# Kernel tuning notes

Measured on AMD Instinct MI355X. Metric: run time of the kernel, lower is better.

## Reference

```python
import jax, jax.numpy as jnp
import numpy as np

N_NODES = 100000
N_EDGES = 1000000
D_IN = 64
D_OUT = 64


def setup_inputs() -> dict:
    key = jax.random.key(0)
    k1, k2, k3, k4 = jax.random.split(key, 4)
    x = jax.random.normal(k1, (N_NODES, D_IN), dtype=jnp.float32)
    edge_index = jax.random.randint(k2, (2, N_EDGES), 0, N_NODES, dtype=jnp.int64)
    edge_weight = jax.random.uniform(k3, (N_EDGES,), dtype=jnp.float32)
    W = jax.random.normal(k4, (D_OUT, D_IN), dtype=jnp.float32) * (1.0 / np.sqrt(D_IN))
    bias = jnp.zeros((D_OUT,), dtype=jnp.float32)
    return {"x": x, "edge_index": edge_index, "edge_weight": edge_weight, "W": W, "bias": bias}


def reference(x, edge_index, edge_weight, W, bias):
    n = x.shape[0]
    self_loops = jnp.arange(n)
    row = jnp.concatenate([edge_index[0], self_loops])  # [E+N]
    col = jnp.concatenate([edge_index[1], self_loops])  # [E+N]
    ew = jnp.concatenate([edge_weight, jnp.ones((n,), x.dtype)])  # [E+N]
    # degree via scatter-add of edge weights into row nodes
    deg = jax.ops.segment_sum(ew, row, num_segments=n)  # [N]
    deg_safe = jnp.where(deg > 0, deg, 1.0)
    deg_inv_sqrt = jnp.where(deg > 0, jax.lax.rsqrt(deg_safe), 0.0)  # inf -> 0
    norm = deg_inv_sqrt[row] * ew * deg_inv_sqrt[col]  # [E+N]
    # gather-scale-scatter aggregation
    msg = x[col] * norm[:, None]  # [E+N, D_IN]
    out = jax.ops.segment_sum(msg, row, num_segments=n)  # [N, D_IN]
    return out @ W.T + bias
```

## Files before the change

kernel.cpp:

```cpp
#include <hip/hip_runtime.h>
#include <hip/hip_bf16.h>

#define D 64
#define K 24
#define M44 ((1ULL << 44) - 1)
#define SPILLCAP 65536

__global__ __launch_bounds__(256) void k_build(const int* __restrict__ rowi,
                                               const int* __restrict__ coli,
                                               const float* __restrict__ ew,
                                               unsigned long long* __restrict__ packed,
                                               unsigned int* __restrict__ slots,
                                               int4* __restrict__ spill,
                                               int* __restrict__ spillCnt, int nE) {
    int e = blockIdx.x * 256 + threadIdx.x;
    if (e >= nE) return;
    int r = rowi[e];
    int c = coli[e];
    float w = ew[e];
    unsigned long long fx = (unsigned long long)((double)w * 4294967296.0);
    unsigned long long old = atomicAdd(&packed[r], (1ULL << 44) | fx);
    int rank = (int)(old >> 44);
    if (rank < K) {
        int q = (int)(w * 32768.0f + 0.5f);
        if (q > 32767) q = 32767;
        slots[r * K + rank] = ((unsigned int)c << 15) | (unsigned int)q;
    } else {
        int p = atomicAdd(spillCnt, 1);
        if (p < SPILLCAP) spill[p] = make_int4(r, c, __float_as_int(w), 0);
    }
}

__global__ __launch_bounds__(256) void k_dis(const unsigned long long* __restrict__ packed,
                                             float* __restrict__ dis,
                                             int* __restrict__ cnt, int n) {
    int i = blockIdx.x * 256 + threadIdx.x;
    if (i >= n) return;
    unsigned long long p = packed[i];
    float dg = (float)(1.0 + (double)(p & M44) * (1.0 / 4294967296.0));
    dis[i] = rsqrtf(dg);
    cnt[i] = (int)(p >> 44);
}

__global__ __launch_bounds__(256) void k_gather_gemm(const float* __restrict__ x,
                                                     const float* __restrict__ dis,
                                                     const int* __restrict__ cnt,
                                                     const unsigned int* __restrict__ slots,
                                                     const int4* __restrict__ spill,
                                                     const int* __restrict__ spillCnt,
                                                     const float* __restrict__ W,
                                                     const float* __restrict__ bias,
                                                     float* __restrict__ out, int n) {
    __shared__ float Bs[D * D];
    __shared__ float Ast[16 * D];
    float4* Ast4 = (float4*)Ast;
    int tid = threadIdx.x;

    const float4* W4 = (const float4*)W;
#pragma unroll
    for (int v = 0; v < 4; ++v) {
        int idx = tid + v * 256;
        int o  = idx >> 4;
        int kc = idx & 15;
        float4 wv = W4[idx];
        int gq = o >> 2, oo = o & 3;
        { int k = 4 * kc + 0; Bs[k * 64 + 4 * ((gq + k) & 15) + oo] = wv.x; }
        { int k = 4 * kc + 1; Bs[k * 64 + 4 * ((gq + k) & 15) + oo] = wv.y; }
        { int k = 4 * kc + 2; Bs[k * 64 + 4 * ((gq + k) & 15) + oo] = wv.z; }
        { int k = 4 * kc + 3; Bs[k * 64 + 4 * ((gq + k) & 15) + oo] = wv.w; }
    }

    int j   = tid & 15;
    int grp = tid >> 4;
    int i0  = blockIdx.x * 16;
    int i   = i0 + grp;

    float4 acc = make_float4(0.f, 0.f, 0.f, 0.f);
    const float4* x4 = (const float4*)x;
    if (i < n) {
        int rawc = cnt[i];
        int c_n = rawc < K ? rawc : K;
        int s = i * K;
        for (int off = 0; off < c_n; off += 16) {
            int idx = off + j;
            unsigned int rec = 0u;
            float wj = 0.f;
            if (idx < c_n) {
                rec = slots[s + idx];
                wj = (float)(rec & 32767u) * (1.0f / 32768.0f) * dis[rec >> 15];
            }
            int mm = c_n - off; if (mm > 16) mm = 16;
#pragma unroll
            for (int t = 0; t < 16; ++t) {
                if (t < mm) {
                    int col = (int)((unsigned int)__shfl((int)rec, t, 16) >> 15);
                    float w = __shfl(wj, t, 16);
                    float4 xv = x4[col * 16 + j];
                    acc.x += w * xv.x; acc.y += w * xv.y;
                    acc.z += w * xv.z; acc.w += w * xv.w;
                }
            }
        }
        if (rawc > K) {
            int total = *spillCnt;
            if (total > SPILLCAP) total = SPILLCAP;
            for (int sp = 0; sp < total; ++sp) {
                int4 v = spill[sp];
                if (v.x == i) {
                    float w = __int_as_float(v.z) * dis[v.y];
                    float4 xv = x4[v.y * 16 + j];
                    acc.x += w * xv.x; acc.y += w * xv.y;
                    acc.z += w * xv.z; acc.w += w * xv.w;
                }
            }
        }
        float di = dis[i];
        float4 xi = x4[i * 16 + j];
        acc.x = di * (di * xi.x + acc.x);
        acc.y = di * (di * xi.y + acc.y);
        acc.z = di * (di * xi.z + acc.z);
        acc.w = di * (di * xi.w + acc.w);
    }
    Ast4[grp * 16 + ((j + (grp >> 2)) & 15)] = acc;
    __syncthreads();

    int row = tid >> 4;
    int cg  = tid & 15;
    float4 oacc = ((const float4*)bias)[cg];
#pragma unroll 4
    for (int kc = 0; kc < 16; ++kc) {
        float4 a4 = Ast4[row * 16 + ((kc + (row >> 2)) & 15)];
        float4 b0 = *(const float4*)&Bs[(4 * kc + 0) * 64 + 4 * ((cg + 4 * kc + 0) & 15)];
        float4 b1 = *(const float4*)&Bs[(4 * kc + 1) * 64 + 4 * ((cg + 4 * kc + 1) & 15)];
        float4 b2 = *(const float4*)&Bs[(4 * kc + 2) * 64 + 4 * ((cg + 4 * kc + 2) & 15)];
        float4 b3 = *(const float4*)&Bs[(4 * kc + 3) * 64 + 4 * ((cg + 4 * kc + 3) & 15)];
        oacc.x += a4.x * b0.x + a4.y * b1.x + a4.z * b2.x + a4.w * b3.x;
        oacc.y += a4.x * b0.y + a4.y * b1.y + a4.z * b2.y + a4.w * b3.y;
        oacc.z += a4.x * b0.z + a4.y * b1.z + a4.z * b2.z + a4.w * b3.z;
        oacc.w += a4.x * b0.w + a4.y * b1.w + a4.z * b2.w + a4.w * b3.w;
    }
    int r = i0 + row;
    if (r < n) ((float4*)out)[r * 16 + cg] = oacc;
}

extern "C" void kernel_launch(void* const* d_in, const int* in_sizes, int n_in,
                              void* d_out, int out_size, void* d_ws, size_t ws_size,
                              hipStream_t stream) {
    const float* x    = (const float*)d_in[0];
    const int*   ei   = (const int*)d_in[1];
    const float* ew   = (const float*)d_in[2];
    const float* W    = (const float*)d_in[3];
    const float* bias = (const float*)d_in[4];
    float* out = (float*)d_out;

    int n  = in_sizes[0] / D;
    int nE = in_sizes[2];
    const int* rowi = ei;
    const int* coli = ei + nE;

    char* w = (char*)d_ws;
    unsigned long long* packed = (unsigned long long*)w; w += (size_t)n * 8;
    int* spillCnt = (int*)w;                             w += 64;
    unsigned int* slots = (unsigned int*)w;              w += (size_t)n * K * 4;
    float* dis = (float*)w;                              w += (size_t)n * 4;
    int*   cnt = (int*)w;                                w += (size_t)n * 4;
    int4*  spill = (int4*)w;

    int gn = (n + 255) / 256;
    int gE = (nE + 255) / 256;
    int gT = (n + 15) / 16;

    hipMemsetAsync(packed, 0, (size_t)n * 8 + 64, stream);
    k_build<<<gE, 256, 0, stream>>>(rowi, coli, ew, packed, slots, spill, spillCnt, nE);
    k_dis  <<<gn, 256, 0, stream>>>(packed, dis, cnt, n);
    k_gather_gemm<<<gT, 256, 0, stream>>>(x, dis, cnt, slots, spill, spillCnt, W, bias, out, n);
}
```

Before: 213.3 us.

## Fuse build, degree and gather-GEMM stages into one cooperative persistent kernel

Replaces the memset plus three separate kernel launches with a single cooperative kernel. It clears the workspace, builds the slot table with atomics, computes degree normalization, and runs the gather plus 64x64 GEMM over persistent tiles, with grid-wide syncs between phases. The goal is to remove per-launch and inter-kernel gaps, and to load W into shared memory once per block instead of once per tile. In exchange it adds grid.sync overhead, caps the grid to occupancy-limited size, and changes how work is spread across blocks. A fallback to the old multi-kernel path remains if the cooperative launch fails.

```diff
diff --git a/kernel.cpp b/kernel.cpp
--- a/kernel.cpp
+++ b/kernel.cpp
@@ -1,10 +1,148 @@
 #include <hip/hip_runtime.h>
+#include <hip/hip_cooperative_groups.h>
 #include <hip/hip_bf16.h>
 
 #define D 64
 #define K 24
 #define M44 ((1ULL << 44) - 1)
 #define SPILLCAP 65536
+
+namespace cg = cooperative_groups;
+
+struct FParams {
+    const float* x; const int* rowi; const int* coli; const float* ew;
+    const float* W; const float* bias; float* out;
+    unsigned long long* packed; int* spillCnt; unsigned int* slots;
+    float* dis; int* cnt; int4* spill;
+    int n; int nE; int ntiles;
+};
+
+__global__ __launch_bounds__(256, 8) void k_fused(FParams p) {
+    cg::grid_group grid = cg::this_grid();
+    __shared__ float Bs[D * D];
+    __shared__ float Ast[16 * D];
+    float4* Ast4 = (float4*)Ast;
+    int tid = threadIdx.x;
+    int gid = blockIdx.x * 256 + tid;
+    int gsz = gridDim.x * 256;
+
+    const float4* W4 = (const float4*)p.W;
+#pragma unroll
+    for (int v = 0; v < 4; ++v) {
+        int idx = tid + v * 256;
+        int o  = idx >> 4;
+        int kc = idx & 15;
+        float4 wv = W4[idx];
+        int gq = o >> 2, oo = o & 3;
+        { int k = 4 * kc + 0; Bs[k * 64 + 4 * ((gq + k) & 15) + oo] = wv.x; }
+        { int k = 4 * kc + 1; Bs[k * 64 + 4 * ((gq + k) & 15) + oo] = wv.y; }
+        { int k = 4 * kc + 2; Bs[k * 64 + 4 * ((gq + k) & 15) + oo] = wv.z; }
+        { int k = 4 * kc + 3; Bs[k * 64 + 4 * ((gq + k) & 15) + oo] = wv.w; }
+    }
+
+    for (int i = gid; i < p.n; i += gsz) p.packed[i] = 0ULL;
+    if (gid == 0) *p.spillCnt = 0;
+    grid.sync();
+
+    for (int e = gid; e < p.nE; e += gsz) {
+        int r = p.rowi[e];
+        int c = p.coli[e];
+        float w = p.ew[e];
+        unsigned long long fx = (unsigned long long)((double)w * 4294967296.0);
+        unsigned long long old = atomicAdd(&p.packed[r], (1ULL << 44) | fx);
+        int rank = (int)(old >> 44);
+        if (rank < K) {
+            int q = (int)(w * 32768.0f + 0.5f);
+            if (q > 32767) q = 32767;
+            p.slots[r * K + rank] = ((unsigned int)c << 15) | (unsigned int)q;
+        } else {
+            int pp = atomicAdd(p.spillCnt, 1);
+            if (pp < SPILLCAP) p.spill[pp] = make_int4(r, c, __float_as_int(w), 0);
+        }
+    }
+    grid.sync();
+
+    for (int i = gid; i < p.n; i += gsz) {
+        unsigned long long pk = p.packed[i];
+        float dg = (float)(1.0 + (double)(pk & M44) * (1.0 / 4294967296.0));
+        p.dis[i] = rsqrtf(dg);
+        p.cnt[i] = (int)(pk >> 44);
+    }
+    grid.sync();
+
+    int j   = tid & 15;
+    int grp = tid >> 4;
+    const float4* x4 = (const float4*)p.x;
+    float4 bv = ((const float4*)p.bias)[j];
+    for (int tile = blockIdx.x; tile < p.ntiles; tile += gridDim.x) {
+        int i0 = tile * 16;
+        int i  = i0 + grp;
+        float4 acc = make_float4(0.f, 0.f, 0.f, 0.f);
+        if (i < p.n) {
+            int rawc = p.cnt[i];
+            int c_n = rawc < K ? rawc : K;
+            int s = i * K;
+            for (int off = 0; off < c_n; off += 16) {
+                int idx = off + j;
+                unsigned int rec = 0u;
+                float wj = 0.f;
+                if (idx < c_n) {
+                    rec = p.slots[s + idx];
+                    wj = (float)(rec & 32767u) * (1.0f / 32768.0f) * p.dis[rec >> 15];
+                }
+                int mm = c_n - off; if (mm > 16) mm = 16;
+#pragma unroll
+                for (int t = 0; t < 16; ++t) {
+                    if (t < mm) {
+                        int col = (int)((unsigned int)__shfl((int)rec, t, 16) >> 15);
+                        float w = __shfl(wj, t, 16);
+                        float4 xv = x4[col * 16 + j];
+                        acc.x += w * xv.x; acc.y += w * xv.y;
+                        acc.z += w * xv.z; acc.w += w * xv.w;
+                    }
+                }
+            }
+            if (rawc > K) {
+                int total = *p.spillCnt;
+                if (total > SPILLCAP) total = SPILLCAP;
+                for (int sp = 0; sp < total; ++sp) {
+                    int4 v = p.spill[sp];
+                    if (v.x == i) {
+                        float w = __int_as_float(v.z) * p.dis[v.y];
+                        float4 xv = x4[v.y * 16 + j];
+                        acc.x += w * xv.x; acc.y += w * xv.y;
+                        acc.z += w * xv.z; acc.w += w * xv.w;
+                    }
+                }
+            }
+            float di = p.dis[i];
+            float4 xi = x4[i * 16 + j];
+            acc.x = di * (di * xi.x + acc.x);
+            acc.y = di * (di * xi.y + acc.y);
+            acc.z = di * (di * xi.z + acc.z);
+            acc.w = di * (di * xi.w + acc.w);
+        }
+        Ast4[grp * 16 + ((j + (grp >> 2)) & 15)] = acc;
+        __syncthreads();
+
+        float4 oacc = bv;
+#pragma unroll 4
+        for (int kc = 0; kc < 16; ++kc) {
+            float4 a4 = Ast4[grp * 16 + ((kc + (grp >> 2)) & 15)];
+            float4 b0 = *(const float4*)&Bs[(4 * kc + 0) * 64 + 4 * ((j + 4 * kc + 0) & 15)];
+            float4 b1 = *(const float4*)&Bs[(4 * kc + 1) * 64 + 4 * ((j + 4 * kc + 1) & 15)];
+            float4 b2 = *(const float4*)&Bs[(4 * kc + 2) * 64 + 4 * ((j + 4 * kc + 2) & 15)];
+            float4 b3 = *(const float4*)&Bs[(4 * kc + 3) * 64 + 4 * ((j + 4 * kc + 3) & 15)];
+            oacc.x += a4.x * b0.x + a4.y * b1.x + a4.z * b2.x + a4.w * b3.x;
+            oacc.y += a4.x * b0.y + a4.y * b1.y + a4.z * b2.y + a4.w * b3.y;
+            oacc.z += a4.x * b0.z + a4.y * b1.z + a4.z * b2.z + a4.w * b3.z;
+            oacc.w += a4.x * b0.w + a4.y * b1.w + a4.z * b2.w + a4.w * b3.w;
+        }
+        int r = i0 + grp;
+        if (r < p.n) ((float4*)p.out)[r * 16 + j] = oacc;
+        __syncthreads();
+    }
+}
 
 __global__ __launch_bounds__(256) void k_build(const int* __restrict__ rowi,
                                                const int* __restrict__ coli,
@@ -124,23 +262,21 @@
     Ast4[grp * 16 + ((j + (grp >> 2)) & 15)] = acc;
     __syncthreads();
 
-    int row = tid >> 4;
-    int cg  = tid & 15;
-    float4 oacc = ((const float4*)bias)[cg];
+    float4 oacc = ((const float4*)bias)[j];
 #pragma unroll 4
     for (int kc = 0; kc < 16; ++kc) {
-        float4 a4 = Ast4[row * 16 + ((kc + (row >> 2)) & 15)];
-        float4 b0 = *(const float4*)&Bs[(4 * kc + 0) * 64 + 4 * ((cg + 4 * kc + 0) & 15)];
-        float4 b1 = *(const float4*)&Bs[(4 * kc + 1) * 64 + 4 * ((cg + 4 * kc + 1) & 15)];
-        float4 b2 = *(const float4*)&Bs[(4 * kc + 2) * 64 + 4 * ((cg + 4 * kc + 2) & 15)];
-        float4 b3 = *(const float4*)&Bs[(4 * kc + 3) * 64 + 4 * ((cg + 4 * kc + 3) & 15)];
+        float4 a4 = Ast4[grp * 16 + ((kc + (grp >> 2)) & 15)];
+        float4 b0 = *(const float4*)&Bs[(4 * kc + 0) * 64 + 4 * ((j + 4 * kc + 0) & 15)];
+        float4 b1 = *(const float4*)&Bs[(4 * kc + 1) * 64 + 4 * ((j + 4 * kc + 1) & 15)];
+        float4 b2 = *(const float4*)&Bs[(4 * kc + 2) * 64 + 4 * ((j + 4 * kc + 2) & 15)];
+        float4 b3 = *(const float4*)&Bs[(4 * kc + 3) * 64 + 4 * ((j + 4 * kc + 3) & 15)];
         oacc.x += a4.x * b0.x + a4.y * b1.x + a4.z * b2.x + a4.w * b3.x;
         oacc.y += a4.x * b0.y + a4.y * b1.y + a4.z * b2.y + a4.w * b3.y;
         oacc.z += a4.x * b0.z + a4.y * b1.z + a4.z * b2.z + a4.w * b3.z;
         oacc.w += a4.x * b0.w + a4.y * b1.w + a4.z * b2.w + a4.w * b3.w;
     }
-    int r = i0 + row;
-    if (r < n) ((float4*)out)[r * 16 + cg] = oacc;
+    int r = i0 + grp;
+    if (r < n) ((float4*)out)[r * 16 + j] = oacc;
 }
 
 extern "C" void kernel_launch(void* const* d_in, const int* in_sizes, int n_in,
@@ -166,12 +302,31 @@
     int*   cnt = (int*)w;                                w += (size_t)n * 4;
     int4*  spill = (int4*)w;
 
-    int gn = (n + 255) / 256;
-    int gE = (nE + 255) / 256;
-    int gT = (n + 15) / 16;
-
-    hipMemsetAsync(packed, 0, (size_t)n * 8 + 64, stream);
-    k_build<<<gE, 256, 0, stream>>>(rowi, coli, ew, packed, slots, spill, spillCnt, nE);
-    k_dis  <<<gn, 256, 0, stream>>>(packed, dis, cnt, n);
-    k_gather_gemm<<<gT, 256, 0, stream>>>(x, dis, cnt, slots, spill, spillCnt, W, bias, out, n);
-}
+    int ntiles = (n + 15) / 16;
+
+    bool coop_done = false;
+    int occ = 0;
+    hipError_t oerr = hipOccupancyMaxActiveBlocksPerMultiprocessor(&occ, k_fused, 256, 0);
+    if (oerr == hipSuccess && occ > 0) {
+        int G = occ * 256;
+        if (G > 2048) G = 2048;
+        FParams p;
+        p.x = x; p.rowi = rowi; p.coli = coli; p.ew = ew; p.W = W; p.bias = bias;
+        p.out = out; p.packed = packed; p.spillCnt = spillCnt; p.slots = slots;
+        p.dis = dis; p.cnt = cnt; p.spill = spill;
+        p.n = n; p.nE = nE; p.ntiles = ntiles;
+        void* args[] = { (void*)&p };
+        hipError_t lerr = hipLaunchCooperativeKernel(k_fused, dim3(G), dim3(256),
+                                                     args, 0, stream);
+        coop_done = (lerr == hipSuccess);
+    }
+
+    if (!coop_done) {
+        int gn = (n + 255) / 256;
+        int gE = (nE + 255) / 256;
+        hipMemsetAsync(packed, 0, (size_t)n * 8 + 64, stream);
+        k_build<<<gE, 256, 0, stream>>>(rowi, coli, ew, packed, slots, spill, spillCnt, nE);
+        k_dis  <<<gn, 256, 0, stream>>>(packed, dis, cnt, n);
+        k_gather_gemm<<<ntiles, 256, 0, stream>>>(x, dis, cnt, slots, spill, spillCnt, W, bias, out, n);
+    }
+}
```

New measurement: 568.0 us. +166.3%, slower.
